# Optimization experiments

Measured on AMD Instinct MI355X. Metric: run time of the kernel, lower is better.

Reference implementation:

```python
import jax, jax.numpy as jnp
import numpy as np
import math
from jax import lax

B, NP1, M, D, H, L, DFF = 16, 65, 256, 512, 8, 3, 2048
EPS_PROJ = 0.01  # MartingaleProjectionLayer is built with epsilon=0.01
LN_EPS = 1e-5


def _pos_encoding(n, d):
    pos = np.arange(n, dtype=np.float32)[:, None]
    div = np.exp(np.arange(0, d, 2, dtype=np.float32) * (-math.log(10000.0) / d))
    pe = np.zeros((n, d), dtype=np.float32)
    pe[:, 0::2] = np.sin(pos * div)
    pe[:, 1::2] = np.cos(pos * div)
    return jnp.asarray(pe)


def setup_inputs() -> dict:
    key = jax.random.key(0)
    ks = jax.random.split(key, 32)
    s = 0.02
    marg = jax.random.uniform(ks[0], (B, NP1, M), jnp.float32)
    marg = marg / marg.sum(axis=-1, keepdims=True)  # proper distributions
    return {
        "marginals": marg,
        "x_grid": jnp.linspace(-3.0, 3.0, M, dtype=jnp.float32),
        "conv_w": jax.random.normal(ks[1], (128, 1, 5), jnp.float32) * s,
        "conv_b": jax.random.normal(ks[2], (128,), jnp.float32) * s,
        "fc_w": jax.random.normal(ks[3], (128, D), jnp.float32) * s,
        "fc_b": jax.random.normal(ks[4], (D,), jnp.float32) * s,
        "ln0_g": jnp.ones((D,), jnp.float32),
        "ln0_b": jnp.zeros((D,), jnp.float32),
        "pos_enc": _pos_encoding(NP1, D),
        "qkv_w": jax.random.normal(ks[5], (L, 3 * D, D), jnp.float32) * s,
        "qkv_b": jax.random.normal(ks[6], (L, 3 * D), jnp.float32) * s,
        "out_w": jax.random.normal(ks[7], (L, D, D), jnp.float32) * s,
        "out_b": jax.random.normal(ks[8], (L, D), jnp.float32) * s,
        "ln1_g": jnp.ones((L, D), jnp.float32),
        "ln1_b": jnp.zeros((L, D), jnp.float32),
        "ff1_w": jax.random.normal(ks[9], (L, DFF, D), jnp.float32) * s,
        "ff1_b": jax.random.normal(ks[10], (L, DFF), jnp.float32) * s,
        "ff2_w": jax.random.normal(ks[11], (L, D, DFF), jnp.float32) * s,
        "ff2_b": jax.random.normal(ks[12], (L, D), jnp.float32) * s,
        "ln2_g": jnp.ones((L, D), jnp.float32),
        "ln2_b": jnp.zeros((L, D), jnp.float32),
        "u_w": jax.random.normal(ks[13], (M, D), jnp.float32) * s,
        "u_b": jax.random.normal(ks[14], (M,), jnp.float32) * s,
        "h_w": jax.random.normal(ks[15], (M, D), jnp.float32) * s,
        "h_b": jax.random.normal(ks[16], (M,), jnp.float32) * s,
    }


def _ln(x, g, b):
    mu = x.mean(axis=-1, keepdims=True)
    var = ((x - mu) ** 2).mean(axis=-1, keepdims=True)
    return (x - mu) * lax.rsqrt(var + LN_EPS) * g + b


def _gelu(x):
    return jax.nn.gelu(x, approximate=False)  # torch default exact GELU


def reference(marginals, x_grid, conv_w, conv_b, fc_w, fc_b, ln0_g, ln0_b,
              pos_enc, qkv_w, qkv_b, out_w, out_b, ln1_g, ln1_b,
              ff1_w, ff1_b, ff2_w, ff2_b, ln2_g, ln2_b, u_w, u_b, h_w, h_b):
    b, np1, m = marginals.shape
    n = np1 - 1
    d = fc_w.shape[1]
    nh = H
    dh = d // nh

    # ---- marginal embedding: Conv1d(1,128,k=5,pad=2) -> mean over grid -> FC+LN+GELU
    x = marginals.reshape(b * np1, 1, m)
    y = lax.conv_general_dilated(x, conv_w, (1,), [(2, 2)],
                                 dimension_numbers=("NCH", "OIH", "NCH"))
    y = y + conv_b[None, :, None]          # (b*np1, 128, m)
    emb = y.mean(axis=2)                   # (b*np1, 128)
    emb = _gelu(_ln(emb @ fc_w + fc_b, ln0_g, ln0_b))
    xs = emb.reshape(b, np1, d) + pos_enc[None, :np1, :]

    # ---- post-norm transformer encoder (dropout off / eval mode)
    scale = 1.0 / math.sqrt(dh)
    for l in range(L):
        qkv = xs @ qkv_w[l].T + qkv_b[l]                        # (b, s, 3d)
        q, k, v = jnp.split(qkv, 3, axis=-1)
        q = q.reshape(b, np1, nh, dh).transpose(0, 2, 1, 3)
        k = k.reshape(b, np1, nh, dh).transpose(0, 2, 1, 3)
        v = v.reshape(b, np1, nh, dh).transpose(0, 2, 1, 3)
        att = jax.nn.softmax(jnp.einsum("bhqd,bhkd->bhqk", q, k) * scale, axis=-1)
        o = jnp.einsum("bhqk,bhkd->bhqd", att, v)
        o = o.transpose(0, 2, 1, 3).reshape(b, np1, d)
        o = o @ out_w[l].T + out_b[l]
        xs = _ln(xs + o, ln1_g[l], ln1_b[l])
        ff = _gelu(xs @ ff1_w[l].T + ff1_b[l]) @ ff2_w[l].T + ff2_b[l]
        xs = _ln(xs + ff, ln2_g[l], ln2_b[l])

    u_pot = xs @ u_w.T + u_b                                    # (b, np1, M)
    h_raw = xs[:, :n, :] @ h_w.T + h_b                          # (b, n, M)

    # ---- vectorized martingale projection over all N timesteps
    x_diff = x_grid[:, None] - x_grid[None, :]                  # (M, M)
    h_kernel = h_raw[..., None] * x_diff                        # (b, n, M, M)
    P = jax.nn.softmax(h_kernel / EPS_PROJ, axis=-1)
    expected_next = jnp.einsum("bnij,j->bni", P, x_grid)
    drift = expected_next - x_grid                              # (b, n, M)
    mu = marginals[:, :n, :]
    weight_drift = (mu * drift).sum(axis=-1, keepdims=True)
    correction = weight_drift / (mu.sum(axis=-1, keepdims=True) + 1e-8)
    h_pot = h_raw - correction
    return (u_pot, h_pot)
```

## Files before the change

### kernel.cpp

```cpp
#include <hip/hip_runtime.h>
#include <math.h>


#define BT   1040
#define NP1  65
#define Dm   512
#define MG   256

typedef short short8 __attribute__((ext_vector_type(8)));
typedef float f32x4  __attribute__((ext_vector_type(4)));
typedef unsigned short u16;

__device__ __forceinline__ u16 f2bf(float f) {
  unsigned int u = __float_as_uint(f);
  u += 0x7FFF + ((u >> 16) & 1);
  return (u16)(u >> 16);
}

__device__ __forceinline__ float gelu_exact(float x) {
  return 0.5f * x * (1.0f + erff(x * 0.70710678118654752f));
}

__device__ __forceinline__ void async16(const u16* g, u16* l) {
  __builtin_amdgcn_global_load_lds(
      (const __attribute__((address_space(1))) unsigned int*)g,
      (__attribute__((address_space(3))) unsigned int*)l, 16, 0, 0);
}

__device__ __forceinline__ float wred(float v) {
#pragma unroll
  for (int o = 32; o; o >>= 1) v += __shfl_xor(v, o, 64);
  return v;
}

__device__ __forceinline__ float block_reduce_sum(float v, float* s) {
#pragma unroll
  for (int off = 32; off; off >>= 1) v += __shfl_down(v, off, 64);
  int lane = threadIdx.x & 63, wid = threadIdx.x >> 6;
  __syncthreads();
  if (lane == 0) s[wid] = v;
  __syncthreads();
  return s[0] + s[1] + s[2] + s[3];
}

__device__ __forceinline__ float f_closed(float a) {
  const float tf = 2.3529411765f;
  float t = a * tf;
  float s = fabsf(t);
  float E;
  if (s < 1e-4f) {
    E = 127.5f - 5461.25f * t;
  } else {
    float u = s * 256.0f;
    float term2 = (u < 80.0f) ? 256.0f / expm1f(u) : 0.0f;
    float Epos = 1.0f / expm1f(s) - term2;
    E = (t > 0.0f) ? Epos : 255.0f - Epos;
  }
  return -3.0f + 0.0235294118f * E;
}

__global__ __launch_bounds__(256) void prep_kernel(
    const float* __restrict__ qkv_w, const float* __restrict__ out_w,
    const float* __restrict__ ff1_w, const float* __restrict__ ff2_w,
    const float* __restrict__ u_w,   const float* __restrict__ h_w,
    u16* __restrict__ wdst,
    const float* __restrict__ marg, const float* __restrict__ conv_w,
    const float* __restrict__ conv_b, const float* __restrict__ fc_w,
    const float* __restrict__ fc_b, const float* __restrict__ g,
    const float* __restrict__ bb, const float* __restrict__ pos,
    float* __restrict__ xs, u16* __restrict__ xsb)
{
  const int tid = threadIdx.x;
  if (blockIdx.x < 512) {
    const size_t O1 = 2359296, O2 = 3145728, O3 = 6291456;
    const size_t O4 = 9437184, O5 = 9568256, TOT4 = 9699328 / 4;
    for (size_t e4 = (size_t)blockIdx.x * 256 + tid; e4 < TOT4;
         e4 += (size_t)512 * 256) {
      size_t e = e4 * 4;
      const float* src;
      if      (e < O1) src = qkv_w + e;
      else if (e < O2) src = out_w + (e - O1);
      else if (e < O3) src = ff1_w + (e - O2);
      else if (e < O4) src = ff2_w + (e - O3);
      else if (e < O5) src = u_w   + (e - O4);
      else             src = h_w   + (e - O5);
      float4 v = *(const float4*)src;
      unsigned int lo = (unsigned int)f2bf(v.x) | ((unsigned int)f2bf(v.y) << 16);
      unsigned int hi = (unsigned int)f2bf(v.z) | ((unsigned int)f2bf(v.w) << 16);
      *(uint2*)(wdst + e) = make_uint2(lo, hi);
    }
    return;
  }
  __shared__ float es[4][128];
  __shared__ float sS[4];
  __shared__ float edge[4][4];
  __shared__ float red[4];
  const int t0 = (blockIdx.x - 512) * 4;
  const int lane = tid & 63, wave = tid >> 6;
  {
    float4 mv = *(const float4*)(marg + (size_t)(t0 + wave) * MG + lane * 4);
    float S = wred(mv.x + mv.y + mv.z + mv.w);
    if (lane == 0) sS[wave] = S;
  }
  if (tid < 16) {
    int k = tid >> 2, e = tid & 3;
    int idx = (e < 2) ? e : (e + 252);
    edge[k][e] = marg[(size_t)(t0 + k) * MG + idx];
  }
  __syncthreads();
  if (tid < 128) {
    int o = tid;
    float w0 = conv_w[o*5+0], w1 = conv_w[o*5+1], w2 = conv_w[o*5+2];
    float w3 = conv_w[o*5+3], w4 = conv_w[o*5+4], cb = conv_b[o];
#pragma unroll
    for (int k = 0; k < 4; ++k) {
      float S = sS[k];
      float x0 = edge[k][0], x1 = edge[k][1], x254 = edge[k][2], x255 = edge[k][3];
      es[k][o] = (w0*(S - x254 - x255) + w1*(S - x255) + w2*S
                + w3*(S - x0) + w4*(S - x0 - x1)) * (1.0f/256.0f) + cb;
    }
  }
  __syncthreads();
  float b0 = fc_b[tid], b1 = fc_b[tid + 256];
  float z[4][2];
#pragma unroll
  for (int k = 0; k < 4; ++k) { z[k][0] = b0; z[k][1] = b1; }
#pragma unroll 4
  for (int o = 0; o < 128; ++o) {
    float f0 = fc_w[(size_t)o*Dm + tid];
    float f1 = fc_w[(size_t)o*Dm + tid + 256];
#pragma unroll
    for (int k = 0; k < 4; ++k) {
      float e = es[k][o];
      z[k][0] += e * f0; z[k][1] += e * f1;
    }
  }
  float g0 = g[tid], g1 = g[tid+256], e0 = bb[tid], e1 = bb[tid+256];
#pragma unroll
  for (int k = 0; k < 4; ++k) {
    float mu = block_reduce_sum(z[k][0] + z[k][1], red) * (1.0f/512.0f);
    float d0 = z[k][0] - mu, d1 = z[k][1] - mu;
    float var = block_reduce_sum(d0*d0 + d1*d1, red) * (1.0f/512.0f);
    float inv = rsqrtf(var + 1e-5f);
    int t = t0 + k, p = t % NP1;
    float y0 = gelu_exact(d0*inv*g0 + e0) + pos[(size_t)p*Dm + tid];
    float y1 = gelu_exact(d1*inv*g1 + e1) + pos[(size_t)p*Dm + tid + 256];
    xs[(size_t)t*Dm + tid]        = y0;
    xs[(size_t)t*Dm + tid + 256]  = y1;
    xsb[(size_t)t*Dm + tid]       = f2bf(y0);
    xsb[(size_t)t*Dm + tid + 256] = f2bf(y1);
  }
}

template<int SPLITS, int MODE>
__global__ __launch_bounds__(256) void gemm_mfma(
    const u16* __restrict__ A, const u16* __restrict__ Bw,
    const float* __restrict__ bias, float* __restrict__ Cf,
    u16* __restrict__ Cb, float* __restrict__ C2,
    const float* __restrict__ bias2, int Mrows, int N, int K)
{
  __shared__ u16 Asl[8*64*8];
  __shared__ u16 Bsl[8*64*8];
  const int tid = threadIdx.x;
  const int row0 = blockIdx.y * 64, col0 = blockIdx.x * 64;
  const int Ks = K / SPLITS, kbase = (int)blockIdx.z * Ks;
  const int lane = tid & 63, wave = tid >> 6;
  const int wm = (wave >> 1) * 32, wn = (wave & 1) * 32;
  const int l15 = lane & 15, q = lane >> 4;

  f32x4 acc[2][2];
  acc[0][0] = (f32x4){0,0,0,0}; acc[0][1] = (f32x4){0,0,0,0};
  acc[1][0] = (f32x4){0,0,0,0}; acc[1][1] = (f32x4){0,0,0,0};

  const int arow = min(row0 + lane, Mrows - 1);
  for (int k0 = kbase; k0 < kbase + Ks; k0 += 64) {
    __syncthreads();
#pragma unroll
    for (int i = 0; i < 2; ++i) {
      int c = wave * 2 + i;
      async16(A + (size_t)arow * K + k0 + c * 8,
              &Asl[(size_t)(c * 64) * 8 + lane * 8]);
      async16(Bw + (size_t)(col0 + lane) * K + k0 + c * 8,
              &Bsl[(size_t)(c * 64) * 8 + lane * 8]);
    }
    __syncthreads();
#pragma unroll
    for (int t = 0; t < 2; ++t) {
      int cc = t * 4 + q;
      short8 af[2], bf[2];
#pragma unroll
      for (int mi = 0; mi < 2; ++mi)
        af[mi] = *(short8*)&Asl[(size_t)(cc*64 + wm + mi*16 + l15) * 8];
#pragma unroll
      for (int ni = 0; ni < 2; ++ni)
        bf[ni] = *(short8*)&Bsl[(size_t)(cc*64 + wn + ni*16 + l15) * 8];
#pragma unroll
      for (int mi = 0; mi < 2; ++mi)
#pragma unroll
        for (int ni = 0; ni < 2; ++ni)
          acc[mi][ni] = __builtin_amdgcn_mfma_f32_16x16x32_bf16(
              af[mi], bf[ni], acc[mi][ni], 0, 0, 0);
    }
  }

  float* Cp = Cf;
  if (MODE == 2) Cp += (size_t)blockIdx.z * (size_t)Mrows * N;
#pragma unroll
  for (int mi = 0; mi < 2; ++mi) {
#pragma unroll
    for (int ni = 0; ni < 2; ++ni) {
      int col = col0 + wn + ni*16 + l15;
#pragma unroll
      for (int r = 0; r < 4; ++r) {
        int row = row0 + wm + mi*16 + q*4 + r;
        if (row < Mrows) {
          float v = acc[mi][ni][r];
          if (MODE == 0) {
            Cp[(size_t)row*N + col] = v + bias[col];
          } else if (MODE == 1) {
            Cb[(size_t)row*N + col] = f2bf(gelu_exact(v + bias[col]));
          } else if (MODE == 2) {
            Cp[(size_t)row*N + col] = v;
          } else {
            if (col < 256) Cf[(size_t)row*256 + col]         = v + bias[col];
            else           C2[(size_t)row*256 + (col - 256)] = v + bias2[col - 256];
          }
        }
      }
    }
  }
}

template<int S>
__global__ __launch_bounds__(256) void add_ln4(
    float* __restrict__ xs, u16* __restrict__ xsb,
    const float* __restrict__ part, const float* __restrict__ bias,
    const float* __restrict__ g, const float* __restrict__ bb)
{
  const int lane = threadIdx.x & 63, wave = threadIdx.x >> 6;
  const int t = blockIdx.x * 4 + wave;
  const int c0 = lane * 8;
  float* xp = xs + (size_t)t * Dm;
  float v[8];
  {
    float4 a0 = *(const float4*)(xp + c0), a1 = *(const float4*)(xp + c0 + 4);
    float4 b0 = *(const float4*)(bias + c0), b1 = *(const float4*)(bias + c0 + 4);
    v[0]=a0.x+b0.x; v[1]=a0.y+b0.y; v[2]=a0.z+b0.z; v[3]=a0.w+b0.w;
    v[4]=a1.x+b1.x; v[5]=a1.y+b1.y; v[6]=a1.z+b1.z; v[7]=a1.w+b1.w;
  }
#pragma unroll
  for (int s = 0; s < S; ++s) {
    const float* pp = part + (size_t)s*BT*Dm + (size_t)t*Dm + c0;
    float4 q0 = *(const float4*)pp, q1 = *(const float4*)(pp + 4);
    v[0]+=q0.x; v[1]+=q0.y; v[2]+=q0.z; v[3]+=q0.w;
    v[4]+=q1.x; v[5]+=q1.y; v[6]+=q1.z; v[7]+=q1.w;
  }
  float s1 = 0.f;
#pragma unroll
  for (int j = 0; j < 8; ++j) s1 += v[j];
  float mu = wred(s1) * (1.0f/512.0f);
  float s2 = 0.f;
#pragma unroll
  for (int j = 0; j < 8; ++j) { float d = v[j]-mu; s2 += d*d; }
  float inv = rsqrtf(wred(s2) * (1.0f/512.0f) + 1e-5f);
  float4 g0 = *(const float4*)(g + c0), g1 = *(const float4*)(g + c0 + 4);
  float4 e0 = *(const float4*)(bb + c0), e1 = *(const float4*)(bb + c0 + 4);
  float gg[8] = {g0.x,g0.y,g0.z,g0.w,g1.x,g1.y,g1.z,g1.w};
  float ee[8] = {e0.x,e0.y,e0.z,e0.w,e1.x,e1.y,e1.z,e1.w};
  float y[8]; u16 yb[8];
#pragma unroll
  for (int j = 0; j < 8; ++j) { y[j] = (v[j]-mu)*inv*gg[j] + ee[j]; yb[j] = f2bf(y[j]); }
  *(float4*)(xp + c0)     = make_float4(y[0],y[1],y[2],y[3]);
  *(float4*)(xp + c0 + 4) = make_float4(y[4],y[5],y[6],y[7]);
  *(short8*)(xsb + (size_t)t*Dm + c0) = *(short8*)yb;
}

__global__ __launch_bounds__(256) void attn_kernel(
    const float* __restrict__ qkv, u16* __restrict__ obufb)
{
  __shared__ float qv[65][67];
  __shared__ float ks[65][67];
  __shared__ float ss[65][67];
  const int b = blockIdx.x >> 3, h = blockIdx.x & 7;
  const int tid = threadIdx.x;
  const float* base = qkv + (size_t)b * NP1 * 1536 + h * 64;
  for (int idx = tid; idx < NP1 * 16; idx += 256) {
    int t = idx >> 4, c = (idx & 15) << 2;
    const float* p = base + (size_t)t * 1536 + c;
    float4 q4 = *(const float4*)(p);
    float4 k4 = *(const float4*)(p + 512);
    qv[t][c] = q4.x; qv[t][c+1] = q4.y; qv[t][c+2] = q4.z; qv[t][c+3] = q4.w;
    ks[t][c] = k4.x; ks[t][c+1] = k4.y; ks[t][c+2] = k4.z; ks[t][c+3] = k4.w;
  }
  __syncthreads();
#pragma unroll
  for (int it = 0; it < 2; ++it) {
    int tile = it * 256 + tid;
    if (tile < 289) {
      int ti = (tile / 17) * 4, tj = (tile % 17) * 4;
      const float* qr[4]; const float* kr[4];
#pragma unroll
      for (int i = 0; i < 4; ++i) { qr[i] = qv[min(ti + i, 64)]; kr[i] = ks[min(tj + i, 64)]; }
      float acc[4][4] = {};
      for (int d = 0; d < 64; ++d) {
        float a[4], bvv[4];
#pragma unroll
        for (int i = 0; i < 4; ++i) { a[i] = qr[i][d]; bvv[i] = kr[i][d]; }
#pragma unroll
        for (int i = 0; i < 4; ++i)
#pragma unroll
          for (int j = 0; j < 4; ++j) acc[i][j] += a[i] * bvv[j];
      }
#pragma unroll
      for (int i = 0; i < 4; ++i)
        if (ti + i < 65)
#pragma unroll
          for (int j = 0; j < 4; ++j)
            if (tj + j < 65) ss[ti + i][tj + j] = acc[i][j] * 0.125f;
    }
  }
  __syncthreads();
  for (int idx = tid; idx < NP1 * 16; idx += 256) {
    int t = idx >> 4, c = (idx & 15) << 2;
    float4 v4 = *(const float4*)(base + (size_t)t * 1536 + 1024 + c);
    qv[t][c] = v4.x; qv[t][c+1] = v4.y; qv[t][c+2] = v4.z; qv[t][c+3] = v4.w;
  }
  if (tid < 65) {
    float mx = -1e30f;
    for (int j = 0; j < 65; ++j) mx = fmaxf(mx, ss[tid][j]);
    float s = 0.0f;
    for (int j = 0; j < 65; ++j) { float e = expf(ss[tid][j] - mx); ss[tid][j] = e; s += e; }
    float inv = 1.0f / s;
    for (int j = 0; j < 65; ++j) ss[tid][j] *= inv;
  }
  __syncthreads();
#pragma unroll
  for (int it = 0; it < 2; ++it) {
    int tile = it * 256 + tid;
    if (tile < 272) {
      int ti = (tile >> 4) * 4, d0 = (tile & 15) * 4;
      const float* sr[4];
#pragma unroll
      for (int i = 0; i < 4; ++i) sr[i] = ss[min(ti + i, 64)];
      float acc[4][4] = {};
      for (int j = 0; j < 65; ++j) {
        float v0 = qv[j][d0], v1 = qv[j][d0+1], v2 = qv[j][d0+2], v3 = qv[j][d0+3];
#pragma unroll
        for (int i = 0; i < 4; ++i) {
          float s = sr[i][j];
          acc[i][0] += s * v0; acc[i][1] += s * v1;
          acc[i][2] += s * v2; acc[i][3] += s * v3;
        }
      }
#pragma unroll
      for (int i = 0; i < 4; ++i)
        if (ti + i < 65) {
          ushort4 o;
          o.x = f2bf(acc[i][0]); o.y = f2bf(acc[i][1]);
          o.z = f2bf(acc[i][2]); o.w = f2bf(acc[i][3]);
          *(ushort4*)(obufb + (size_t)(b * NP1 + ti + i) * Dm + h * 64 + d0) = o;
        }
    }
  }
}

__global__ __launch_bounds__(256) void proj_closed(
    const float* __restrict__ hbuf, const float* __restrict__ marg,
    const float* __restrict__ xg, float* __restrict__ out_h)
{
  const int tid = threadIdx.x, lane = tid & 63, wave = tid >> 6;
  const int rr = blockIdx.x * 4 + wave;
  const int b = rr >> 6, n = rr & 63;
  const int row = b * NP1 + n;
  const int i0 = lane * 4;
  float4 a4 = *(const float4*)(hbuf + (size_t)row * MG + i0);
  float4 x4 = *(const float4*)(xg + i0);
  float4 m4 = *(const float4*)(marg + (size_t)row * MG + i0);
  float av[4] = {a4.x, a4.y, a4.z, a4.w};
  float xv[4] = {x4.x, x4.y, x4.z, x4.w};
  float uv[4] = {m4.x, m4.y, m4.z, m4.w};
  float wd = 0.f, ms = 0.f;
#pragma unroll
  for (int k = 0; k < 4; ++k) {
    float drift = f_closed(av[k]) - xv[k];
    wd += uv[k] * drift; ms += uv[k];
  }
  wd = wred(wd); ms = wred(ms);
  float corr = wd / (ms + 1e-8f);
  *(float4*)(out_h + ((size_t)(b * 64 + n)) * MG + i0) =
      make_float4(av[0]-corr, av[1]-corr, av[2]-corr, av[3]-corr);
}

extern "C" void kernel_launch(void* const* d_in, const int* in_sizes, int n_in,
                              void* d_out, int out_size, void* d_ws, size_t ws_size,
                              hipStream_t stream)
{
  const float* marg   = (const float*)d_in[0];
  const float* xg     = (const float*)d_in[1];
  const float* conv_w = (const float*)d_in[2];
  const float* conv_b = (const float*)d_in[3];
  const float* fc_w   = (const float*)d_in[4];
  const float* fc_b   = (const float*)d_in[5];
  const float* ln0_g  = (const float*)d_in[6];
  const float* ln0_b  = (const float*)d_in[7];
  const float* pos    = (const float*)d_in[8];
  const float* qkv_w  = (const float*)d_in[9];
  const float* qkv_b  = (const float*)d_in[10];
  const float* out_w  = (const float*)d_in[11];
  const float* out_b  = (const float*)d_in[12];
  const float* ln1_g  = (const float*)d_in[13];
  const float* ln1_b  = (const float*)d_in[14];
  const float* ff1_w  = (const float*)d_in[15];
  const float* ff1_b  = (const float*)d_in[16];
  const float* ff2_w  = (const float*)d_in[17];
  const float* ff2_b  = (const float*)d_in[18];
  const float* ln2_g  = (const float*)d_in[19];
  const float* ln2_b  = (const float*)d_in[20];
  const float* u_w    = (const float*)d_in[21];
  const float* u_b    = (const float*)d_in[22];
  const float* h_w    = (const float*)d_in[23];
  const float* h_b    = (const float*)d_in[24];
  float* out = (float*)d_out;

  float* ws = (float*)d_ws;
  float* xs      = ws;
  float* qkvbuf  = ws + 532480;
  float* part    = ws + 2129920;
  float* hbuf    = ws + 4259840;
  u16*   xsb     = (u16*)(ws + 4526080);
  u16*   obufb   = (u16*)(ws + 4792320);
  u16*   ffb     = (u16*)(ws + 5058560);
  u16*   wbf     = (u16*)(ws + 6123520);

  const u16* qkv_bw = wbf;
  const u16* out_bw = wbf + 2359296;
  const u16* ff1_bw = wbf + 3145728;
  const u16* ff2_bw = wbf + 6291456;
  const u16* uh_bw  = wbf + 9437184;

  prep_kernel<<<772, 256, 0, stream>>>(
      qkv_w, out_w, ff1_w, ff2_w, u_w, h_w, wbf,
      marg, conv_w, conv_b, fc_w, fc_b, ln0_g, ln0_b, pos, xs, xsb);

  for (int l = 0; l < 3; ++l) {
    gemm_mfma<1,0><<<dim3(24, 17), 256, 0, stream>>>(
        xsb, qkv_bw + (size_t)l*786432, qkv_b + l*1536, qkvbuf,
        nullptr, nullptr, nullptr, BT, 1536, 512);
    attn_kernel<<<128, 256, 0, stream>>>(qkvbuf, obufb);
    gemm_mfma<2,2><<<dim3(8, 17, 2), 256, 0, stream>>>(
        obufb, out_bw + (size_t)l*262144, nullptr, part,
        nullptr, nullptr, nullptr, BT, 512, 512);
    add_ln4<2><<<260, 256, 0, stream>>>(xs, xsb, part, out_b + l*512,
                                        ln1_g + l*512, ln1_b + l*512);
    gemm_mfma<1,1><<<dim3(32, 17), 256, 0, stream>>>(
        xsb, ff1_bw + (size_t)l*1048576, ff1_b + l*2048, nullptr,
        ffb, nullptr, nullptr, BT, 2048, 512);
    gemm_mfma<4,2><<<dim3(8, 17, 4), 256, 0, stream>>>(
        ffb, ff2_bw + (size_t)l*1048576, nullptr, part,
        nullptr, nullptr, nullptr, BT, 512, 2048);
    add_ln4<4><<<260, 256, 0, stream>>>(xs, xsb, part, ff2_b + l*512,
                                        ln2_g + l*512, ln2_b + l*512);
  }

  gemm_mfma<1,3><<<dim3(8, 17), 256, 0, stream>>>(
      xsb, uh_bw, u_b, out, nullptr, hbuf, h_b, BT, 512, 512);
  proj_closed<<<256, 256, 0, stream>>>(hbuf, marg, xg, out + 1040*256);
}
```

Before: 406.1 us.

## Double-buffer LDS tiles in MFMA GEMM to overlap loads with compute

Gives the bf16 MFMA GEMM two LDS buffers for the A and B tiles. The async global-to-LDS load for the next K-slice is issued before computing the current one, using explicit vmcnt waits and raw barriers, so memory latency overlaps the MFMA work. This doubles LDS use per block, which may lower occupancy. Relying on manual waitcnt with the raw s_barrier intrinsic is fragile if the compiler emits extra loads.

```diff
diff --git a/kernel.cpp b/kernel.cpp
--- a/kernel.cpp
+++ b/kernel.cpp
@@ -159,8 +159,8 @@
     u16* __restrict__ Cb, float* __restrict__ C2,
     const float* __restrict__ bias2, int Mrows, int N, int K)
 {
-  __shared__ u16 Asl[8*64*8];
-  __shared__ u16 Bsl[8*64*8];
+  __shared__ u16 Asl[2][8*64*8];
+  __shared__ u16 Bsl[2][8*64*8];
   const int tid = threadIdx.x;
   const int row0 = blockIdx.y * 64, col0 = blockIdx.x * 64;
   const int Ks = K / SPLITS, kbase = (int)blockIdx.z * Ks;
@@ -173,27 +173,44 @@
   acc[1][0] = (f32x4){0,0,0,0}; acc[1][1] = (f32x4){0,0,0,0};
 
   const int arow = min(row0 + lane, Mrows - 1);
-  for (int k0 = kbase; k0 < kbase + Ks; k0 += 64) {
-    __syncthreads();
-#pragma unroll
-    for (int i = 0; i < 2; ++i) {
-      int c = wave * 2 + i;
-      async16(A + (size_t)arow * K + k0 + c * 8,
-              &Asl[(size_t)(c * 64) * 8 + lane * 8]);
-      async16(Bw + (size_t)(col0 + lane) * K + k0 + c * 8,
-              &Bsl[(size_t)(c * 64) * 8 + lane * 8]);
-    }
-    __syncthreads();
-#pragma unroll
-    for (int t = 0; t < 2; ++t) {
-      int cc = t * 4 + q;
+  const size_t abase = (size_t)arow * K;
+  const size_t bbase = (size_t)(col0 + lane) * K;
+  const int c0w = wave * 2;
+
+#pragma unroll
+  for (int i = 0; i < 2; ++i) {
+    int c = c0w + i;
+    async16(A + abase + kbase + c * 8, &Asl[0][(size_t)(c * 64 + lane) * 8]);
+    async16(Bw + bbase + kbase + c * 8, &Bsl[0][(size_t)(c * 64 + lane) * 8]);
+  }
+
+  const int nk = Ks >> 6;
+  for (int t = 0; t < nk; ++t) {
+    const int cur = t & 1;
+    if (t + 1 < nk) {
+      const int nxt = cur ^ 1;
+      const int kk = kbase + (t + 1) * 64;
+#pragma unroll
+      for (int i = 0; i < 2; ++i) {
+        int c = c0w + i;
+        async16(A + abase + kk + c * 8, &Asl[nxt][(size_t)(c * 64 + lane) * 8]);
+        async16(Bw + bbase + kk + c * 8, &Bsl[nxt][(size_t)(c * 64 + lane) * 8]);
+      }
+      asm volatile("s_waitcnt vmcnt(4)" ::: "memory");
+    } else {
+      asm volatile("s_waitcnt vmcnt(0)" ::: "memory");
+    }
+    __builtin_amdgcn_s_barrier();
+#pragma unroll
+    for (int tt = 0; tt < 2; ++tt) {
+      int cc = tt * 4 + q;
       short8 af[2], bf[2];
 #pragma unroll
       for (int mi = 0; mi < 2; ++mi)
-        af[mi] = *(short8*)&Asl[(size_t)(cc*64 + wm + mi*16 + l15) * 8];
+        af[mi] = *(short8*)&Asl[cur][(size_t)(cc*64 + wm + mi*16 + l15) * 8];
 #pragma unroll
       for (int ni = 0; ni < 2; ++ni)
-        bf[ni] = *(short8*)&Bsl[(size_t)(cc*64 + wn + ni*16 + l15) * 8];
+        bf[ni] = *(short8*)&Bsl[cur][(size_t)(cc*64 + wn + ni*16 + l15) * 8];
 #pragma unroll
       for (int mi = 0; mi < 2; ++mi)
 #pragma unroll
@@ -201,6 +218,7 @@
           acc[mi][ni] = __builtin_amdgcn_mfma_f32_16x16x32_bf16(
               af[mi], bf[ni], acc[mi][ni], 0, 0, 0);
     }
+    __builtin_amdgcn_s_barrier();
   }
 
   float* Cp = Cf;
```

Measured after the change: 405.4 us. No clear change (-0.2%).
